# Kernel optimization log

Measured on AMD Instinct MI355X. Metric: run time of the kernel, lower is better.

The kernel has to match this reference:

```python
import jax, jax.numpy as jnp
import numpy as np

EMBED = 768
HEADS = 12
HEAD_DIM = EMBED // HEADS
HIDDEN = 4 * EMBED
EPS = 1e-5


def setup_inputs() -> dict:
    key = jax.random.key(0)
    ks = jax.random.split(key, 12)
    s = lambda fan_in: 1.0 / np.sqrt(fan_in)
    return {
        "x": jax.random.normal(ks[0], (4, 2048, EMBED), dtype=jnp.float32),
        "ln1_g": jnp.ones((EMBED,), jnp.float32),
        "ln1_b": jnp.zeros((EMBED,), jnp.float32),
        "qkv_w": jax.random.normal(ks[1], (EMBED, 3 * EMBED), jnp.float32) * s(EMBED),
        "qkv_b": jnp.zeros((3 * EMBED,), jnp.float32),
        "proj_w": jax.random.normal(ks[2], (EMBED, EMBED), jnp.float32) * s(EMBED),
        "proj_b": jnp.zeros((EMBED,), jnp.float32),
        "ln2_g": jnp.ones((EMBED,), jnp.float32),
        "ln2_b": jnp.zeros((EMBED,), jnp.float32),
        "fc1_w": jax.random.normal(ks[3], (EMBED, HIDDEN), jnp.float32) * s(EMBED),
        "fc1_b": jnp.zeros((HIDDEN,), jnp.float32),
        "fc2_w": jax.random.normal(ks[4], (HIDDEN, EMBED), jnp.float32) * s(HIDDEN),
        "fc2_b": jnp.zeros((EMBED,), jnp.float32),
    }


def _layernorm(x, g, b):
    mu = jnp.mean(x, axis=-1, keepdims=True)
    var = jnp.var(x, axis=-1, keepdims=True)
    return (x - mu) * jax.lax.rsqrt(var + EPS) * g + b


def reference(x, ln1_g, ln1_b, qkv_w, qkv_b, proj_w, proj_b,
              ln2_g, ln2_b, fc1_w, fc1_b, fc2_w, fc2_b):
    B, N, C = x.shape
    # --- attention (pre-LN) ---
    xn = _layernorm(x, ln1_g, ln1_b)
    qkv = xn @ qkv_w + qkv_b                       # [B,N,3C]
    qkv = qkv.reshape(B, N, 3, HEADS, HEAD_DIM)
    q, k, v = jnp.moveaxis(qkv, 2, 0)              # each [B,N,H,D]
    q = jnp.swapaxes(q, 1, 2)                      # [B,H,N,D]
    k = jnp.swapaxes(k, 1, 2)
    v = jnp.swapaxes(v, 1, 2)
    scale = HEAD_DIM ** -0.5
    attn = jax.nn.softmax(jnp.einsum('bhnd,bhmd->bhnm', q, k) * scale, axis=-1)
    out = jnp.einsum('bhnm,bhmd->bhnd', attn, v)   # [B,H,N,D]
    out = jnp.swapaxes(out, 1, 2).reshape(B, N, C)
    out = out @ proj_w + proj_b
    x = x + out
    # --- MLP (pre-LN) ---
    xn2 = _layernorm(x, ln2_g, ln2_b)
    h = jax.nn.gelu(xn2 @ fc1_w + fc1_b, approximate=False)
    x = x + (h @ fc2_w + fc2_b)
    return x
```

## Files before the change

kernel.cpp:

```cpp
#include <hip/hip_runtime.h>

typedef unsigned short ushort_t;
typedef __attribute__((ext_vector_type(8))) unsigned short ushort8;
typedef __attribute__((ext_vector_type(4))) unsigned short ushort4v;
typedef __attribute__((ext_vector_type(2))) unsigned int uint2v;
typedef __attribute__((ext_vector_type(4))) float f32x4;
typedef __attribute__((ext_vector_type(8))) __bf16 bf16x8;

#define DEVFN static __device__ __forceinline__

DEVFN unsigned short f2bf(float f) {
    unsigned int u = __builtin_bit_cast(unsigned int, f);
    u += 0x7FFFu + ((u >> 16) & 1u);
    return (unsigned short)(u >> 16);
}

DEVFN bf16x8 ldsfrag(const ushort_t* p) {
    ushort8 u = *reinterpret_cast<const ushort8*>(p);
    return __builtin_bit_cast(bf16x8, u);
}

DEVFN bf16x8 ldg8(const ushort_t* p) {
    ushort8 u = *reinterpret_cast<const ushort8*>(p);
    return __builtin_bit_cast(bf16x8, u);
}

DEVFN f32x4 mfma16(bf16x8 a, bf16x8 b, f32x4 c) {
    return __builtin_amdgcn_mfma_f32_16x16x32_bf16(a, b, c, 0, 0, 0);
}

DEVFN void gl2lds16(const ushort_t* g, ushort_t* l) {
    __builtin_amdgcn_global_load_lds(
        (const __attribute__((address_space(1))) unsigned int*)g,
        (__attribute__((address_space(3))) unsigned int*)l, 16, 0, 0);
}

DEVFN unsigned int cvtpk(float lo, float hi) {
    unsigned int r;
    asm("v_cvt_pk_bf16_f32 %0, %1, %2" : "=v"(r) : "v"(lo), "v"(hi));
    return r;
}

DEVFN float gelu_fast(float v) {
    const float a = 0.7978845608f * v * fmaf(0.044715f, v * v, 1.0f);
    const float e = __builtin_amdgcn_exp2f(2.885390082f * a);
    const float th = 1.0f - 2.0f * __builtin_amdgcn_rcpf(e + 1.0f);
    return 0.5f * v * (1.0f + th);
}

__global__ __launch_bounds__(256) void wt4_kernel(
    const float* __restrict__ qkv_w, const float* __restrict__ proj_w,
    const float* __restrict__ fc1_w, const float* __restrict__ fc2_w,
    ushort_t* __restrict__ qkv_wt, ushort_t* __restrict__ proj_wt,
    ushort_t* __restrict__ fc1_wt, ushort_t* __restrict__ fc2_wt) {
    __shared__ float t[32][33];
    const int bid = blockIdx.x;
    const float* in; ushort_t* out; int K, N, n0, k0;
    if (bid < 1728)      { in = qkv_w;  out = qkv_wt;  K = 768;  N = 2304;
                           n0 = (bid % 72) * 32;  k0 = (bid / 72) * 32; }
    else if (bid < 2304) { const int r = bid - 1728; in = proj_w; out = proj_wt;
                           K = 768;  N = 768;
                           n0 = (r % 24) * 32;    k0 = (r / 24) * 32; }
    else if (bid < 4608) { const int r = bid - 2304; in = fc1_w;  out = fc1_wt;
                           K = 768;  N = 3072;
                           n0 = (r % 96) * 32;    k0 = (r / 96) * 32; }
    else                 { const int r = bid - 4608; in = fc2_w;  out = fc2_wt;
                           K = 3072; N = 768;
                           n0 = (r % 24) * 32;    k0 = (r / 24) * 32; }
    const int tx = threadIdx.x & 31, ty = threadIdx.x >> 5;
    for (int j = 0; j < 4; j++)
        t[ty + 8 * j][tx] = in[(size_t)(k0 + ty + 8 * j) * N + n0 + tx];
    __syncthreads();
    for (int j = 0; j < 4; j++)
        out[(size_t)(n0 + ty + 8 * j) * K + k0 + tx] = f2bf(t[tx][ty + 8 * j]);
}

__global__ __launch_bounds__(256) void ln_kernel(const float* __restrict__ x,
                                                 const float* __restrict__ g,
                                                 const float* __restrict__ bta,
                                                 ushort_t* __restrict__ out) {
    const int row = blockIdx.x;
    const int tid = threadIdx.x;
    const float* xr = x + (size_t)row * 768;
    float v0 = xr[tid], v1 = xr[tid + 256], v2 = xr[tid + 512];
    float s = v0 + v1 + v2;
    float q = v0 * v0 + v1 * v1 + v2 * v2;
    for (int d = 32; d; d >>= 1) {
        s += __shfl_down(s, d);
        q += __shfl_down(q, d);
    }
    __shared__ float red[8];
    const int w = tid >> 6, lane = tid & 63;
    if (lane == 0) { red[w] = s; red[4 + w] = q; }
    __syncthreads();
    if (tid == 0) {
        float ts = red[0] + red[1] + red[2] + red[3];
        float tq = red[4] + red[5] + red[6] + red[7];
        float mu = ts * (1.0f / 768.0f);
        float var = tq * (1.0f / 768.0f) - mu * mu;
        red[0] = mu;
        red[1] = rsqrtf(var + 1e-5f);
    }
    __syncthreads();
    const float mu = red[0], rs = red[1];
    ushort_t* orow = out + (size_t)row * 768;
    orow[tid]       = f2bf((v0 - mu) * rs * g[tid]       + bta[tid]);
    orow[tid + 256] = f2bf((v1 - mu) * rs * g[tid + 256] + bta[tid + 256]);
    orow[tid + 512] = f2bf((v2 - mu) * rs * g[tid + 512] + bta[tid + 512]);
}

enum { EPI_QKV = 0, EPI_RES = 1, EPI_GELU = 2 };

template <int EPI, int BN, int BK>
__global__ __launch_bounds__(256) void gemm_kernel(
    const ushort_t* __restrict__ A, const ushort_t* __restrict__ BT,
    const float* __restrict__ bias, const float* __restrict__ resid,
    float* __restrict__ outf, ushort_t* __restrict__ outb,
    ushort_t* __restrict__ vtout, int M, int N, int K) {
    constexpr int NT = BN / 32;
    constexpr int SL = BK / 8;
    constexpr int SM = SL - 1;
    constexpr int RPI = 64 / SL;
    constexpr int AI = 128 / RPI / 4;
    constexpr int BI = BN / RPI / 4;
    __shared__ __align__(16) ushort_t As[2][128 * BK];
    __shared__ __align__(16) ushort_t Bs[2][BN * BK];
    const int bn = blockIdx.x, bm = blockIdx.y;
    const int tid = threadIdx.x;
    const int lane = tid & 63, w = tid >> 6;
    const int wm = (w >> 1) * 64, wn = (w & 1) * (BN / 2);
    const int l15 = lane & 15, l4 = lane >> 4;

    const int srow = lane / SL;
    const int scol = ((lane & SM) ^ (srow & SM)) * 8;
    const ushort_t* gA = A + (size_t)(bm * 128 + w * (AI * RPI) + srow) * K + scol;
    const ushort_t* gB = BT + (size_t)(bn * BN + w * (BI * RPI) + srow) * K + scol;

    const int swm = l15 & SM;
    int aoff[BK / 32], boff[BK / 32];
#pragma unroll
    for (int kk = 0; kk < BK / 32; kk++) {
        aoff[kk] = (wm + l15) * BK + ((((kk << 2) | l4) ^ swm) * 8);
        boff[kk] = (wn + l15) * BK + ((((kk << 2) | l4) ^ swm) * 8);
    }

    f32x4 acc[4][NT] = {};

    auto stage = [&](int k0, int buf) {
#pragma unroll
        for (int i = 0; i < AI; i++)
            gl2lds16(gA + k0 + i * RPI * K, &As[buf][(w * AI + i) * 512]);
#pragma unroll
        for (int i = 0; i < BI; i++)
            gl2lds16(gB + k0 + i * RPI * K, &Bs[buf][(w * BI + i) * 512]);
    };

    stage(0, 0);
    __syncthreads();
    int cur = 0;
    for (int k0 = 0; k0 < K; k0 += BK) {
        if (k0 + BK < K) stage(k0 + BK, cur ^ 1);
#pragma unroll
        for (int kk = 0; kk < BK / 32; kk++) {
            bf16x8 af[4], bfr[NT];
#pragma unroll
            for (int mt = 0; mt < 4; mt++)
                af[mt] = ldsfrag(As[cur] + aoff[kk] + mt * 16 * BK);
#pragma unroll
            for (int nt = 0; nt < NT; nt++)
                bfr[nt] = ldsfrag(Bs[cur] + boff[kk] + nt * 16 * BK);
#pragma unroll
            for (int mt = 0; mt < 4; mt++)
#pragma unroll
                for (int nt = 0; nt < NT; nt++)
                    acc[mt][nt] = mfma16(bfr[nt], af[mt], acc[mt][nt]);
        }
        __syncthreads();
        cur ^= 1;
    }

#pragma unroll
    for (int nt = 0; nt < NT; nt++) {
        const int gc0 = bn * BN + wn + nt * 16 + l4 * 4;
        const f32x4 bi = *reinterpret_cast<const f32x4*>(bias + gc0);
#pragma unroll
        for (int mt = 0; mt < 4; mt++) {
            const int gr = bm * 128 + wm + mt * 16 + l15;
            f32x4 v = acc[mt][nt] + bi;
            if constexpr (EPI == EPI_QKV) {
                if (gc0 < 768) v *= 0.18033688011f;
                if (gc0 >= 1536) {
                    const int d = gc0 - 1536;
                    const int h = d >> 6, dh = d & 63;
                    const int b = gr >> 11, tl = gr & 2047;
                    ushort_t* vrow = vtout + ((size_t)((b * 12 + h) * 64 + dh)) * 2048 + tl;
                    vrow[0]        = f2bf(v[0]);
                    vrow[2048]     = f2bf(v[1]);
                    vrow[2 * 2048] = f2bf(v[2]);
                    vrow[3 * 2048] = f2bf(v[3]);
                } else {
                    uint2v o;
                    o[0] = cvtpk(v[0], v[1]);
                    o[1] = cvtpk(v[2], v[3]);
                    *reinterpret_cast<uint2v*>(outb + (size_t)gr * N + gc0) = o;
                }
            } else if constexpr (EPI == EPI_RES) {
                const f32x4 rsd = *reinterpret_cast<const f32x4*>(resid + (size_t)gr * N + gc0);
                *reinterpret_cast<f32x4*>(outf + (size_t)gr * N + gc0) = v + rsd;
            } else {
                f32x4 gl;
#pragma unroll
                for (int r = 0; r < 4; r++) gl[r] = gelu_fast(v[r]);
                uint2v o;
                o[0] = cvtpk(gl[0], gl[1]);
                o[1] = cvtpk(gl[2], gl[3]);
                *reinterpret_cast<uint2v*>(outb + (size_t)gr * N + gc0) = o;
            }
        }
    }
}

__global__ __launch_bounds__(256, 4) void attn_kernel(const ushort_t* __restrict__ qkv,
                                                      const ushort_t* __restrict__ vt,
                                                      ushort_t* __restrict__ out) {
    __shared__ __align__(16) ushort_t Kb[2][4096];
    __shared__ __align__(16) ushort_t Vb[2][4096];
    __shared__ __align__(16) ushort_t Ps[4][1024];

    const int bid = blockIdx.x;
    const int nid = (bid & 7) * 192 + (bid >> 3);
    const int qt = nid & 31;
    const int bh = nid >> 5;
    const int b = bh / 12, h = bh % 12;
    const int tid = threadIdx.x;
    const int lane = tid & 63, w = tid >> 6;
    const int l15 = lane & 15, l4 = lane >> 4;

    const ushort_t* qrow = qkv + (size_t)(b * 2048 + qt * 64 + w * 16 + l15) * 2304 + h * 64;
    const bf16x8 aq0 = ldg8(qrow + l4 * 8);
    const bf16x8 aq1 = ldg8(qrow + 32 + l4 * 8);

    const int jr0 = w * 16 + (lane >> 3);
    const int jr1 = jr0 + 8;
    const int c0 = ((lane & 7) ^ (jr0 & 7)) * 8;
    const int c1 = ((lane & 7) ^ (jr1 & 7)) * 8;
    const ushort_t* kg0 = qkv + (size_t)(b * 2048 + jr0) * 2304 + 768 + h * 64 + c0;
    const ushort_t* kg1 = qkv + (size_t)(b * 2048 + jr1) * 2304 + 768 + h * 64 + c1;
    const ushort_t* vg0 = vt + (size_t)(bh * 64 + jr0) * 2048 + c0;
    const ushort_t* vg1 = vt + (size_t)(bh * 64 + jr1) * 2048 + c1;

    const int sw7 = l15 & 7;
    const int ka0 = l15 * 64 + ((l4 ^ sw7) * 8);
    const int ka1 = l15 * 64 + (((4 + l4) ^ sw7) * 8);

    ushort_t* const psw = Ps[w];
    const int pw_m = l15 & 14;
    int pwoff[4];
#pragma unroll
    for (int jt = 0; jt < 4; jt++) pwoff[jt] = l15 * 64 + (((jt * 4 + l4) ^ pw_m) * 4);
    const int pr0 = l15 * 64 + (((2 * l4) ^ pw_m) * 4);
    const int pr1 = l15 * 64 + (((8 + 2 * l4) ^ pw_m) * 4);

    float lrun = 0.f;
    f32x4 oacc[4] = {};

    gl2lds16(kg0, &Kb[0][w * 1024]);
    gl2lds16(kg1, &Kb[0][w * 1024 + 512]);
    gl2lds16(vg0, &Vb[0][w * 1024]);
    gl2lds16(vg1, &Vb[0][w * 1024 + 512]);
    __syncthreads();

    for (int kt = 0; kt < 32; kt++) {
        const int cur = kt & 1;
        if (kt < 31) {
            const size_t ko = (size_t)(kt + 1) * 64 * 2304;
            const int vo = (kt + 1) * 64;
            gl2lds16(kg0 + ko, &Kb[cur ^ 1][w * 1024]);
            gl2lds16(kg1 + ko, &Kb[cur ^ 1][w * 1024 + 512]);
            gl2lds16(vg0 + vo, &Vb[cur ^ 1][w * 1024]);
            gl2lds16(vg1 + vo, &Vb[cur ^ 1][w * 1024 + 512]);
        }
        const ushort_t* kb = Kb[cur];
        const ushort_t* vb = Vb[cur];

        f32x4 st[4];
        __builtin_amdgcn_s_setprio(1);
#pragma unroll
        for (int jt = 0; jt < 4; jt++) {
            f32x4 z = {};
            z = mfma16(ldsfrag(kb + ka0 + jt * 1024), aq0, z);
            z = mfma16(ldsfrag(kb + ka1 + jt * 1024), aq1, z);
            st[jt] = z;
        }
        __builtin_amdgcn_s_setprio(0);

        float rs = 0.f;
#pragma unroll
        for (int jt = 0; jt < 4; jt++) {
            const float p0 = __builtin_amdgcn_exp2f(st[jt][0]);
            const float p1 = __builtin_amdgcn_exp2f(st[jt][1]);
            const float p2 = __builtin_amdgcn_exp2f(st[jt][2]);
            const float p3 = __builtin_amdgcn_exp2f(st[jt][3]);
            rs += (p0 + p1) + (p2 + p3);
            uint2v pw;
            pw[0] = cvtpk(p0, p1);
            pw[1] = cvtpk(p2, p3);
            *reinterpret_cast<uint2v*>(psw + pwoff[jt]) = pw;
        }
        lrun += rs;

        const bf16x8 pf0 = ldsfrag(psw + pr0);
        const bf16x8 pf1 = ldsfrag(psw + pr1);

        __builtin_amdgcn_s_setprio(1);
#pragma unroll
        for (int dt = 0; dt < 4; dt++) {
            const bf16x8 vf0 = ldsfrag(vb + ka0 + dt * 1024);
            const bf16x8 vf1 = ldsfrag(vb + ka1 + dt * 1024);
            oacc[dt] = mfma16(vf0, pf0, oacc[dt]);
            oacc[dt] = mfma16(vf1, pf1, oacc[dt]);
        }
        __builtin_amdgcn_s_setprio(0);
        __syncthreads();
    }

    lrun += __shfl_xor(lrun, 16);
    lrun += __shfl_xor(lrun, 32);
    const float linv = __builtin_amdgcn_rcpf(lrun);

    ushort_t* orow = out + (size_t)(b * 2048 + qt * 64 + w * 16 + l15) * 768 + h * 64 + l4 * 4;
#pragma unroll
    for (int dt = 0; dt < 4; dt++) {
        ushort4v o;
#pragma unroll
        for (int r = 0; r < 4; r++) o[r] = f2bf(oacc[dt][r] * linv);
        *reinterpret_cast<ushort4v*>(orow + dt * 16) = o;
    }
}

extern "C" void kernel_launch(void* const* d_in, const int* in_sizes, int n_in,
                              void* d_out, int out_size, void* d_ws, size_t ws_size,
                              hipStream_t stream) {
    const float* x      = (const float*)d_in[0];
    const float* ln1_g  = (const float*)d_in[1];
    const float* ln1_b  = (const float*)d_in[2];
    const float* qkv_w  = (const float*)d_in[3];
    const float* qkv_b  = (const float*)d_in[4];
    const float* proj_w = (const float*)d_in[5];
    const float* proj_b = (const float*)d_in[6];
    const float* ln2_g  = (const float*)d_in[7];
    const float* ln2_b  = (const float*)d_in[8];
    const float* fc1_w  = (const float*)d_in[9];
    const float* fc1_b  = (const float*)d_in[10];
    const float* fc2_w  = (const float*)d_in[11];
    const float* fc2_b  = (const float*)d_in[12];
    float* out = (float*)d_out;

    char* ws = (char*)d_ws;
    ushort_t* qkv_wt  = (ushort_t*)(ws);
    ushort_t* proj_wt = (ushort_t*)(ws + 3538944);
    ushort_t* fc1_wt  = (ushort_t*)(ws + 4718592);
    ushort_t* fc2_wt  = (ushort_t*)(ws + 9437184);
    ushort_t* xb      = (ushort_t*)(ws + 14155776);
    ushort_t* aob     = (ushort_t*)(ws + 26738688);
    ushort_t* qkvb    = (ushort_t*)(ws + 39321600);
    ushort_t* vtb     = (ushort_t*)(ws + 77070336);
    ushort_t* hb      = (ushort_t*)(ws + 39321600);

    dim3 blk(256);

    wt4_kernel<<<dim3(6912), blk, 0, stream>>>(qkv_w, proj_w, fc1_w, fc2_w,
                                               qkv_wt, proj_wt, fc1_wt, fc2_wt);
    ln_kernel<<<8192, blk, 0, stream>>>(x, ln1_g, ln1_b, xb);
    gemm_kernel<EPI_QKV, 128, 32><<<dim3(18, 64), blk, 0, stream>>>(
        xb, qkv_wt, qkv_b, nullptr, nullptr, qkvb, vtb, 8192, 2304, 768);
    attn_kernel<<<dim3(1536), blk, 0, stream>>>(qkvb, vtb, aob);
    gemm_kernel<EPI_RES, 64, 64><<<dim3(12, 64), blk, 0, stream>>>(
        aob, proj_wt, proj_b, x, out, nullptr, nullptr, 8192, 768, 768);
    ln_kernel<<<8192, blk, 0, stream>>>(out, ln2_g, ln2_b, xb);
    gemm_kernel<EPI_GELU, 128, 32><<<dim3(24, 64), blk, 0, stream>>>(
        xb, fc1_wt, fc1_b, nullptr, nullptr, hb, nullptr, 8192, 3072, 768);
    gemm_kernel<EPI_RES, 64, 64><<<dim3(12, 64), blk, 0, stream>>>(
        hb, fc2_wt, fc2_b, out, out, nullptr, nullptr, 8192, 768, 3072);
}
```

Measured before the change: 313.8 us.

## Keep softmax probabilities in registers and use 16x16x16 MFMA for PV

```diff
diff --git a/kernel.cpp b/kernel.cpp
--- a/kernel.cpp
+++ b/kernel.cpp
@@ -20,6 +20,10 @@
     return __builtin_bit_cast(bf16x8, u);
 }
 
+DEVFN uint2v ld64u(const ushort_t* p) {
+    return *reinterpret_cast<const uint2v*>(p);
+}
+
 DEVFN bf16x8 ldg8(const ushort_t* p) {
     ushort8 u = *reinterpret_cast<const ushort8*>(p);
     return __builtin_bit_cast(bf16x8, u);
@@ -27,6 +31,10 @@
 
 DEVFN f32x4 mfma16(bf16x8 a, bf16x8 b, f32x4 c) {
     return __builtin_amdgcn_mfma_f32_16x16x32_bf16(a, b, c, 0, 0, 0);
+}
+
+DEVFN void mfmaPV(uint2v a, uint2v b, f32x4& c) {
+    asm("v_mfma_f32_16x16x16_bf16 %0, %1, %2, %0" : "+v"(c) : "v"(a), "v"(b));
 }
 
 DEVFN void gl2lds16(const ushort_t* g, ushort_t* l) {
@@ -220,12 +228,11 @@
     }
 }
 
-__global__ __launch_bounds__(256, 4) void attn_kernel(const ushort_t* __restrict__ qkv,
+__global__ __launch_bounds__(256, 5) void attn_kernel(const ushort_t* __restrict__ qkv,
                                                       const ushort_t* __restrict__ vt,
                                                       ushort_t* __restrict__ out) {
     __shared__ __align__(16) ushort_t Kb[2][4096];
     __shared__ __align__(16) ushort_t Vb[2][4096];
-    __shared__ __align__(16) ushort_t Ps[4][1024];
 
     const int bid = blockIdx.x;
     const int nid = (bid & 7) * 192 + (bid >> 3);
@@ -252,14 +259,10 @@
     const int sw7 = l15 & 7;
     const int ka0 = l15 * 64 + ((l4 ^ sw7) * 8);
     const int ka1 = l15 * 64 + (((4 + l4) ^ sw7) * 8);
-
-    ushort_t* const psw = Ps[w];
-    const int pw_m = l15 & 14;
-    int pwoff[4];
-#pragma unroll
-    for (int jt = 0; jt < 4; jt++) pwoff[jt] = l15 * 64 + (((jt * 4 + l4) ^ pw_m) * 4);
-    const int pr0 = l15 * 64 + (((2 * l4) ^ pw_m) * 4);
-    const int pr1 = l15 * 64 + (((8 + 2 * l4) ^ pw_m) * 4);
+    int voffj[4];
+#pragma unroll
+    for (int jt = 0; jt < 4; jt++)
+        voffj[jt] = (((jt * 2 + (l4 >> 1)) ^ sw7) * 8) + (l4 & 1) * 4;
 
     float lrun = 0.f;
     f32x4 oacc[4] = {};
@@ -295,6 +298,7 @@
         __builtin_amdgcn_s_setprio(0);
 
         float rs = 0.f;
+        uint2v pk[4];
 #pragma unroll
         for (int jt = 0; jt < 4; jt++) {
             const float p0 = __builtin_amdgcn_exp2f(st[jt][0]);
@@ -302,27 +306,24 @@
             const float p2 = __builtin_amdgcn_exp2f(st[jt][2]);
             const float p3 = __builtin_amdgcn_exp2f(st[jt][3]);
             rs += (p0 + p1) + (p2 + p3);
-            uint2v pw;
-            pw[0] = cvtpk(p0, p1);
-            pw[1] = cvtpk(p2, p3);
-            *reinterpret_cast<uint2v*>(psw + pwoff[jt]) = pw;
+            pk[jt][0] = cvtpk(p0, p1);
+            pk[jt][1] = cvtpk(p2, p3);
         }
         lrun += rs;
 
-        const bf16x8 pf0 = ldsfrag(psw + pr0);
-        const bf16x8 pf1 = ldsfrag(psw + pr1);
-
+        const ushort_t* vrow = vb + l15 * 64;
+        asm volatile("s_nop 1");
         __builtin_amdgcn_s_setprio(1);
 #pragma unroll
-        for (int dt = 0; dt < 4; dt++) {
-            const bf16x8 vf0 = ldsfrag(vb + ka0 + dt * 1024);
-            const bf16x8 vf1 = ldsfrag(vb + ka1 + dt * 1024);
-            oacc[dt] = mfma16(vf0, pf0, oacc[dt]);
-            oacc[dt] = mfma16(vf1, pf1, oacc[dt]);
-        }
+        for (int jt = 0; jt < 4; jt++)
+#pragma unroll
+            for (int dt = 0; dt < 4; dt++)
+                mfmaPV(ld64u(vrow + dt * 1024 + voffj[jt]), pk[jt], oacc[dt]);
         __builtin_amdgcn_s_setprio(0);
         __syncthreads();
     }
+
+    asm volatile("s_nop 7\ns_nop 7");
 
     lrun += __shfl_xor(lrun, 16);
     lrun += __shfl_xor(lrun, 32);
@@ -331,10 +332,10 @@
     ushort_t* orow = out + (size_t)(b * 2048 + qt * 64 + w * 16 + l15) * 768 + h * 64 + l4 * 4;
 #pragma unroll
     for (int dt = 0; dt < 4; dt++) {
-        ushort4v o;
-#pragma unroll
-        for (int r = 0; r < 4; r++) o[r] = f2bf(oacc[dt][r] * linv);
-        *reinterpret_cast<ushort4v*>(orow + dt * 16) = o;
+        uint2v o;
+        o[0] = cvtpk(oacc[dt][0] * linv, oacc[dt][1] * linv);
+        o[1] = cvtpk(oacc[dt][2] * linv, oacc[dt][3] * linv);
+        *reinterpret_cast<uint2v*>(orow + dt * 16) = o;
     }
 }
 
```

Measured after the change: 317.1 us. About the same (+1.1%).

## Merge weight transpose with first layernorm and remap GEMM block order for XCDs

Applied to the files above, without the earlier changes.

```diff
diff --git a/kernel.cpp b/kernel.cpp
--- a/kernel.cpp
+++ b/kernel.cpp
@@ -48,13 +48,48 @@
     return 0.5f * v * (1.0f + th);
 }
 
-__global__ __launch_bounds__(256) void wt4_kernel(
+__global__ __launch_bounds__(256) void prep_kernel(
     const float* __restrict__ qkv_w, const float* __restrict__ proj_w,
     const float* __restrict__ fc1_w, const float* __restrict__ fc2_w,
     ushort_t* __restrict__ qkv_wt, ushort_t* __restrict__ proj_wt,
-    ushort_t* __restrict__ fc1_wt, ushort_t* __restrict__ fc2_wt) {
+    ushort_t* __restrict__ fc1_wt, ushort_t* __restrict__ fc2_wt,
+    const float* __restrict__ x, const float* __restrict__ ln1_g,
+    const float* __restrict__ ln1_b, ushort_t* __restrict__ xb) {
     __shared__ float t[32][33];
     const int bid = blockIdx.x;
+    const int tid = threadIdx.x;
+
+    if (bid >= 6912) {
+        const int row = bid - 6912;
+        const float* xr = x + (size_t)row * 768;
+        float v0 = xr[tid], v1 = xr[tid + 256], v2 = xr[tid + 512];
+        float s = v0 + v1 + v2;
+        float q = v0 * v0 + v1 * v1 + v2 * v2;
+        for (int d = 32; d; d >>= 1) {
+            s += __shfl_down(s, d);
+            q += __shfl_down(q, d);
+        }
+        float* red = &t[0][0];
+        const int w = tid >> 6, lane = tid & 63;
+        if (lane == 0) { red[w] = s; red[4 + w] = q; }
+        __syncthreads();
+        if (tid == 0) {
+            float ts = red[0] + red[1] + red[2] + red[3];
+            float tq = red[4] + red[5] + red[6] + red[7];
+            float mu = ts * (1.0f / 768.0f);
+            float var = tq * (1.0f / 768.0f) - mu * mu;
+            red[0] = mu;
+            red[1] = rsqrtf(var + 1e-5f);
+        }
+        __syncthreads();
+        const float mu = red[0], rs = red[1];
+        ushort_t* orow = xb + (size_t)row * 768;
+        orow[tid]       = f2bf((v0 - mu) * rs * ln1_g[tid]       + ln1_b[tid]);
+        orow[tid + 256] = f2bf((v1 - mu) * rs * ln1_g[tid + 256] + ln1_b[tid + 256]);
+        orow[tid + 512] = f2bf((v2 - mu) * rs * ln1_g[tid + 512] + ln1_b[tid + 512]);
+        return;
+    }
+
     const float* in; ushort_t* out; int K, N, n0, k0;
     if (bid < 1728)      { in = qkv_w;  out = qkv_wt;  K = 768;  N = 2304;
                            n0 = (bid % 72) * 32;  k0 = (bid / 72) * 32; }
@@ -67,7 +102,7 @@
     else                 { const int r = bid - 4608; in = fc2_w;  out = fc2_wt;
                            K = 3072; N = 768;
                            n0 = (r % 24) * 32;    k0 = (r / 24) * 32; }
-    const int tx = threadIdx.x & 31, ty = threadIdx.x >> 5;
+    const int tx = tid & 31, ty = tid >> 5;
     for (int j = 0; j < 4; j++)
         t[ty + 8 * j][tx] = in[(size_t)(k0 + ty + 8 * j) * N + n0 + tx];
     __syncthreads();
@@ -125,7 +160,11 @@
     constexpr int BI = BN / RPI / 4;
     __shared__ __align__(16) ushort_t As[2][128 * BK];
     __shared__ __align__(16) ushort_t Bs[2][BN * BK];
-    const int bn = blockIdx.x, bm = blockIdx.y;
+    const int id = blockIdx.x;
+    const int nbn = gridDim.x >> 6;
+    const int p = id >> 3;
+    const int bn = p % nbn;
+    const int bm = (id & 7) * 8 + p / nbn;
     const int tid = threadIdx.x;
     const int lane = tid & 63, w = tid >> 6;
     const int wm = (w >> 1) * 64, wn = (w & 1) * (BN / 2);
@@ -369,17 +408,17 @@
 
     dim3 blk(256);
 
-    wt4_kernel<<<dim3(6912), blk, 0, stream>>>(qkv_w, proj_w, fc1_w, fc2_w,
-                                               qkv_wt, proj_wt, fc1_wt, fc2_wt);
-    ln_kernel<<<8192, blk, 0, stream>>>(x, ln1_g, ln1_b, xb);
-    gemm_kernel<EPI_QKV, 128, 32><<<dim3(18, 64), blk, 0, stream>>>(
+    prep_kernel<<<dim3(15104), blk, 0, stream>>>(qkv_w, proj_w, fc1_w, fc2_w,
+                                                 qkv_wt, proj_wt, fc1_wt, fc2_wt,
+                                                 x, ln1_g, ln1_b, xb);
+    gemm_kernel<EPI_QKV, 128, 32><<<dim3(18 * 64), blk, 0, stream>>>(
         xb, qkv_wt, qkv_b, nullptr, nullptr, qkvb, vtb, 8192, 2304, 768);
     attn_kernel<<<dim3(1536), blk, 0, stream>>>(qkvb, vtb, aob);
-    gemm_kernel<EPI_RES, 64, 64><<<dim3(12, 64), blk, 0, stream>>>(
+    gemm_kernel<EPI_RES, 64, 64><<<dim3(12 * 64), blk, 0, stream>>>(
         aob, proj_wt, proj_b, x, out, nullptr, nullptr, 8192, 768, 768);
     ln_kernel<<<8192, blk, 0, stream>>>(out, ln2_g, ln2_b, xb);
-    gemm_kernel<EPI_GELU, 128, 32><<<dim3(24, 64), blk, 0, stream>>>(
+    gemm_kernel<EPI_GELU, 128, 32><<<dim3(24 * 64), blk, 0, stream>>>(
         xb, fc1_wt, fc1_b, nullptr, nullptr, hb, nullptr, 8192, 3072, 768);
-    gemm_kernel<EPI_RES, 64, 64><<<dim3(12, 64), blk, 0, stream>>>(
+    gemm_kernel<EPI_RES, 64, 64><<<dim3(12 * 64), blk, 0, stream>>>(
         hb, fc2_wt, fc2_b, out, out, nullptr, nullptr, 8192, 768, 3072);
 }
```

Result: faster. 282.6 us (-9.9%).
